# Performance work log

Hardware: AMD Instinct MI355X
Metric: run time of the kernel (lower is better)

## Reference

```python
import jax, jax.numpy as jnp
import numpy as np

DELTA_V = 0.5
DELTA_D = 3.0
ALPHA = 1.0
BETA = 1.0
GAMMA = 0.001
K = 5  # max instance label (labels 1..K; 0 = background)


def setup_inputs() -> dict:
    key = jax.random.key(0)
    k1, k2 = jax.random.split(key)
    B, D, H, W = 8, 8, 512, 1024
    embedding = jax.random.normal(k1, (B, D, H, W), dtype=jnp.float32)
    instance_mask = jax.random.randint(k2, (B, H, W), 0, K + 1, dtype=jnp.int32)
    return {"embedding": embedding, "instance_mask": instance_mask}


def _disc_loss(embedding, instance_mask):
    B, D, H, W = embedding.shape
    P = H * W
    emb = embedding.transpose(0, 2, 3, 1).reshape(B, P, D)      # [B,P,D]
    labels = instance_mask.reshape(B, P)                         # [B,P]

    # one-hot over instance labels 1..K (background excluded)
    onehot = (labels[..., None] == jnp.arange(1, K + 1, dtype=labels.dtype)).astype(emb.dtype)  # [B,P,K]
    counts = onehot.sum(axis=1)                                  # [B,K]
    present = counts > 0                                         # [B,K]
    presentf = present.astype(emb.dtype)
    N = presentf.sum(axis=-1)                                    # [B] num instances

    # per-instance centers via segment mean
    sums = jnp.einsum('bpd,bpk->bkd', emb, onehot)               # [B,K,D]
    centers = sums / jnp.maximum(counts, 1.0)[..., None]         # [B,K,D]

    # ---- variance loss: per-pixel distance to own center ----
    idx = jnp.clip(labels - 1, 0, K - 1)                         # [B,P]
    c_pix = jnp.take_along_axis(centers, idx[..., None], axis=1) # [B,P,D]
    d = jnp.sqrt(jnp.sum((emb - c_pix) ** 2, axis=-1))           # [B,P]
    val = jnp.maximum(d - DELTA_V, 0.0) ** 2                     # [B,P]
    inst_sum = jnp.einsum('bp,bpk->bk', val, onehot)             # [B,K]
    inst_mean = inst_sum / jnp.maximum(counts, 1.0)
    loss_var_b = (inst_mean * presentf).sum(-1) / jnp.maximum(N, 1.0)  # [B]

    # ---- distance loss: pairwise center hinge ----
    diff = centers[:, :, None, :] - centers[:, None, :, :]       # [B,K,K,D]
    dist_sq = jnp.sum(diff ** 2, axis=-1)                        # [B,K,K]
    iu = jnp.triu(jnp.ones((K, K), dtype=bool), k=1)             # i<j
    pair_mask = present[:, :, None] & present[:, None, :] & iu   # [B,K,K]
    safe_dist = jnp.sqrt(jnp.where(pair_mask, dist_sq, 1.0))
    term = jnp.maximum(2.0 * DELTA_D - safe_dist, 0.0) ** 2 * pair_mask.astype(emb.dtype)
    n_pairs = N * (N - 1.0) / 2.0
    loss_dist_b = term.sum((-1, -2)) / jnp.where(N > 1, n_pairs, 1.0)  # [B]

    # ---- regularization: mean norm of present centers ----
    c_norm = jnp.sqrt(jnp.where(present, jnp.sum(centers ** 2, axis=-1), 1.0))
    loss_reg_b = (c_norm * presentf).sum(-1) / jnp.maximum(N, 1.0)     # [B]

    # ---- batch mean over images that have at least one instance ----
    has = (N > 0).astype(emb.dtype)                              # [B]
    denom = jnp.maximum(has.sum(), 1.0)
    loss_var = (loss_var_b * has).sum() / denom
    loss_dist = (loss_dist_b * has).sum() / denom
    loss_reg = (loss_reg_b * has).sum() / denom
    total = ALPHA * loss_var + BETA * loss_dist + GAMMA * loss_reg
    return (total, loss_var, loss_dist, loss_reg)


def reference(embedding, instance_mask):
    return _disc_loss(embedding, instance_mask)
```

## Files before the change

### kernel.cpp

```cpp
#include <hip/hip_runtime.h>
#include <math.h>

constexpr int NB   = 8;
constexpr int ND   = 8;
constexpr int NH   = 512;
constexpr int NW   = 1024;
constexpr int NP   = NH * NW;
constexpr int NG   = NP / 4;
constexpr int NK   = 5;
constexpr int BPB  = 128;
constexpr int GPB  = NG / BPB;
constexpr int NVAL = NK * ND + NK;

constexpr float DELTA_V = 0.5f;
constexpr float TWO_DELTA_D = 6.0f;
constexpr float GAMMA = 0.001f;

__device__ __forceinline__ float wave_sum(float v) {
#pragma unroll
    for (int off = 32; off > 0; off >>= 1) v += __shfl_down(v, off, 64);
    return v;
}

__global__ __launch_bounds__(256) void pass1_kernel(const float* __restrict__ emb,
                                                    const int* __restrict__ mask,
                                                    float* __restrict__ sums,
                                                    float* __restrict__ cnts) {
    const int b   = blockIdx.x / BPB;
    const int blk = blockIdx.x % BPB;
    const long base = (long)blk * GPB;

    const float4* emb4 = (const float4*)emb;
    const int4*   m4p  = (const int4*)mask + (long)b * NG;

    float acc[NK][ND];
    float cnt[NK];
#pragma unroll
    for (int k = 0; k < NK; ++k) {
        cnt[k] = 0.f;
#pragma unroll
        for (int d = 0; d < ND; ++d) acc[k][d] = 0.f;
    }

    for (int it = threadIdx.x; it < GPB; it += blockDim.x) {
        const long g = base + it;
        const int4 m = m4p[g];
        float4 e[ND];
#pragma unroll
        for (int d = 0; d < ND; ++d)
            e[d] = emb4[((long)(b * ND + d)) * NG + g];
        const int labs[4] = {m.x, m.y, m.z, m.w};
#pragma unroll
        for (int j = 0; j < 4; ++j) {
            const int lab = labs[j];
#pragma unroll
            for (int k = 0; k < NK; ++k) {
                const float is = (lab == k + 1) ? 1.f : 0.f;
                cnt[k] += is;
#pragma unroll
                for (int d = 0; d < ND; ++d)
                    acc[k][d] = fmaf(is, ((const float*)&e[d])[j], acc[k][d]);
            }
        }
    }

    __shared__ float part[4][NVAL];
    const int lane = threadIdx.x & 63;
    const int wave = threadIdx.x >> 6;
#pragma unroll
    for (int k = 0; k < NK; ++k) {
#pragma unroll
        for (int d = 0; d < ND; ++d) {
            const float r = wave_sum(acc[k][d]);
            if (lane == 0) part[wave][k * ND + d] = r;
        }
        const float rc = wave_sum(cnt[k]);
        if (lane == 0) part[wave][NK * ND + k] = rc;
    }
    __syncthreads();
    if (threadIdx.x < NVAL) {
        const float s = part[0][threadIdx.x] + part[1][threadIdx.x] +
                        part[2][threadIdx.x] + part[3][threadIdx.x];
        if (threadIdx.x < NK * ND)
            atomicAdd(&sums[b * NK * ND + threadIdx.x], s);
        else
            atomicAdd(&cnts[b * NK + (threadIdx.x - NK * ND)], s);
    }
}

__global__ __launch_bounds__(256) void pass2_kernel(const float* __restrict__ emb,
                                                    const int* __restrict__ mask,
                                                    const float* __restrict__ sums,
                                                    const float* __restrict__ cnts,
                                                    float* __restrict__ vsums) {
    const int b   = blockIdx.x / BPB;
    const int blk = blockIdx.x % BPB;
    const long base = (long)blk * GPB;

    float c[NK][ND];
#pragma unroll
    for (int k = 0; k < NK; ++k) {
        const float inv = 1.f / fmaxf(cnts[b * NK + k], 1.f);
#pragma unroll
        for (int d = 0; d < ND; ++d)
            c[k][d] = sums[b * NK * ND + k * ND + d] * inv;
    }

    const float4* emb4 = (const float4*)emb;
    const int4*   m4p  = (const int4*)mask + (long)b * NG;

    float vacc[NK] = {0.f, 0.f, 0.f, 0.f, 0.f};

    for (int it = threadIdx.x; it < GPB; it += blockDim.x) {
        const long g = base + it;
        const int4 m = m4p[g];
        float4 e[ND];
#pragma unroll
        for (int d = 0; d < ND; ++d)
            e[d] = emb4[((long)(b * ND + d)) * NG + g];
        const int labs[4] = {m.x, m.y, m.z, m.w};
#pragma unroll
        for (int j = 0; j < 4; ++j) {
            const int lab = labs[j];
            float dsq = 0.f;
#pragma unroll
            for (int d = 0; d < ND; ++d) {
                float cd = c[0][d];
                cd = (lab == 2) ? c[1][d] : cd;
                cd = (lab == 3) ? c[2][d] : cd;
                cd = (lab == 4) ? c[3][d] : cd;
                cd = (lab == 5) ? c[4][d] : cd;
                const float diff = ((const float*)&e[d])[j] - cd;
                dsq = fmaf(diff, diff, dsq);
            }
            const float dist = sqrtf(dsq);
            float hv = fmaxf(dist - DELTA_V, 0.f);
            const float val = hv * hv;
#pragma unroll
            for (int k = 0; k < NK; ++k)
                vacc[k] += (lab == k + 1) ? val : 0.f;
        }
    }

    __shared__ float part[4][NK];
    const int lane = threadIdx.x & 63;
    const int wave = threadIdx.x >> 6;
#pragma unroll
    for (int k = 0; k < NK; ++k) {
        const float r = wave_sum(vacc[k]);
        if (lane == 0) part[wave][k] = r;
    }
    __syncthreads();
    if (threadIdx.x < NK) {
        const float s = part[0][threadIdx.x] + part[1][threadIdx.x] +
                        part[2][threadIdx.x] + part[3][threadIdx.x];
        atomicAdd(&vsums[b * NK + threadIdx.x], s);
    }
}

__global__ void final_kernel(const float* __restrict__ sums,
                             const float* __restrict__ cnts,
                             const float* __restrict__ vsums,
                             float* __restrict__ out) {
    if (threadIdx.x != 0 || blockIdx.x != 0) return;
    float tv = 0.f, td = 0.f, tr = 0.f, hs = 0.f;
    for (int b = 0; b < NB; ++b) {
        float cnt[NK];
        bool  pres[NK];
        float c[NK][ND];
        float N = 0.f;
        for (int k = 0; k < NK; ++k) {
            cnt[k]  = cnts[b * NK + k];
            pres[k] = cnt[k] > 0.f;
            if (pres[k]) N += 1.f;
            const float inv = 1.f / fmaxf(cnt[k], 1.f);
            for (int d = 0; d < ND; ++d)
                c[k][d] = sums[b * NK * ND + k * ND + d] * inv;
        }
        float lv = 0.f;
        for (int k = 0; k < NK; ++k)
            if (pres[k]) lv += vsums[b * NK + k] / fmaxf(cnt[k], 1.f);
        lv /= fmaxf(N, 1.f);
        float ld = 0.f;
        for (int i = 0; i < NK; ++i)
            for (int j = i + 1; j < NK; ++j)
                if (pres[i] && pres[j]) {
                    float dsq = 0.f;
                    for (int d = 0; d < ND; ++d) {
                        const float df = c[i][d] - c[j][d];
                        dsq = fmaf(df, df, dsq);
                    }
                    const float t = fmaxf(TWO_DELTA_D - sqrtf(dsq), 0.f);
                    ld += t * t;
                }
        const float npairs = N * (N - 1.f) * 0.5f;
        ld /= (N > 1.f) ? npairs : 1.f;
        float lr = 0.f;
        for (int k = 0; k < NK; ++k)
            if (pres[k]) {
                float sq = 0.f;
                for (int d = 0; d < ND; ++d) sq = fmaf(c[k][d], c[k][d], sq);
                lr += sqrtf(sq);
            }
        lr /= fmaxf(N, 1.f);

        if (N > 0.f) { tv += lv; td += ld; tr += lr; hs += 1.f; }
    }
    const float denom = fmaxf(hs, 1.f);
    tv /= denom; td /= denom; tr /= denom;
    out[0] = tv + td + GAMMA * tr;
    out[1] = tv;
    out[2] = td;
    out[3] = tr;
}

extern "C" void kernel_launch(void* const* d_in, const int* in_sizes, int n_in,
                              void* d_out, int out_size, void* d_ws, size_t ws_size,
                              hipStream_t stream) {
    const float* emb  = (const float*)d_in[0];
    const int*   mask = (const int*)d_in[1];
    float* out = (float*)d_out;

    float* sums  = (float*)d_ws;
    float* cnts  = sums + NB * NK * ND;
    float* vsums = cnts + NB * NK;

    hipMemsetAsync(d_ws, 0, (size_t)(NB * NK * ND + 2 * NB * NK) * sizeof(float), stream);

    dim3 grid(NB * BPB), block(256);
    pass1_kernel<<<grid, block, 0, stream>>>(emb, mask, sums, cnts);
    pass2_kernel<<<grid, block, 0, stream>>>(emb, mask, sums, cnts, vsums);
    final_kernel<<<1, 64, 0, stream>>>(sums, cnts, vsums, out);
}
```

Measured before the change: 286.1 us.

## Fuse both passes and final reduction into one cooperative kernel with grid sync

Replaces the memset plus three kernel launches with a single cooperative kernel of 512 blocks that uses grid.sync between phases. Per-block partials are written to workspace and reduced deterministically instead of through atomics. Block 0 finishes with a per-image final loss computed in parallel. This removes launch and memset overhead, but halves the block count, and grid-wide barriers add synchronisation cost. Both passes still read the embedding in full, with no reuse across them.

```diff
diff --git a/kernel.cpp b/kernel.cpp
--- a/kernel.cpp
+++ b/kernel.cpp
@@ -1,5 +1,8 @@
 #include <hip/hip_runtime.h>
+#include <hip/hip_cooperative_groups.h>
 #include <math.h>
+
+namespace cg = cooperative_groups;
 
 constexpr int NB   = 8;
 constexpr int ND   = 8;
@@ -7,14 +10,15 @@
 constexpr int NW   = 1024;
 constexpr int NP   = NH * NW;
 constexpr int NG   = NP / 4;
+constexpr int BPB  = 64;
+constexpr int NBLK = NB * BPB;
+constexpr int GPB  = NG / BPB;
 constexpr int NK   = 5;
-constexpr int BPB  = 128;
-constexpr int GPB  = NG / BPB;
 constexpr int NVAL = NK * ND + NK;
 
-constexpr float DELTA_V = 0.5f;
+constexpr float DELTA_V     = 0.5f;
 constexpr float TWO_DELTA_D = 6.0f;
-constexpr float GAMMA = 0.001f;
+constexpr float GAMMA       = 0.001f;
 
 __device__ __forceinline__ float wave_sum(float v) {
 #pragma unroll
@@ -22,17 +26,30 @@
     return v;
 }
 
-__global__ __launch_bounds__(256) void pass1_kernel(const float* __restrict__ emb,
-                                                    const int* __restrict__ mask,
-                                                    float* __restrict__ sums,
-                                                    float* __restrict__ cnts) {
+__global__ __launch_bounds__(256, 2) void fused_kernel(
+        const float* __restrict__ emb,
+        const int*   __restrict__ mask,
+        float* __restrict__ part1,
+        float* __restrict__ gcent,
+        float* __restrict__ gcnt,
+        float* __restrict__ part2,
+        float* __restrict__ out) {
+    const cg::grid_group grid = cg::this_grid();
     const int b   = blockIdx.x / BPB;
     const int blk = blockIdx.x % BPB;
     const long base = (long)blk * GPB;
+    const int lane = threadIdx.x & 63;
+    const int wave = threadIdx.x >> 6;
 
     const float4* emb4 = (const float4*)emb;
     const int4*   m4p  = (const int4*)mask + (long)b * NG;
 
+    __shared__ float part[4][NVAL];
+    __shared__ float red[NVAL];
+    __shared__ float csh[NK][ND];
+    __shared__ float vsh[NB][NK];
+    __shared__ float bl[4][NB];
+
     float acc[NK][ND];
     float cnt[NK];
 #pragma unroll
@@ -42,7 +59,7 @@
         for (int d = 0; d < ND; ++d) acc[k][d] = 0.f;
     }
 
-    for (int it = threadIdx.x; it < GPB; it += blockDim.x) {
+    for (int it = threadIdx.x; it < GPB; it += 256) {
         const long g = base + it;
         const int4 m = m4p[g];
         float4 e[ND];
@@ -64,9 +81,6 @@
         }
     }
 
-    __shared__ float part[4][NVAL];
-    const int lane = threadIdx.x & 63;
-    const int wave = threadIdx.x >> 6;
 #pragma unroll
     for (int k = 0; k < NK; ++k) {
 #pragma unroll
@@ -79,39 +93,39 @@
     }
     __syncthreads();
     if (threadIdx.x < NVAL) {
-        const float s = part[0][threadIdx.x] + part[1][threadIdx.x] +
-                        part[2][threadIdx.x] + part[3][threadIdx.x];
-        if (threadIdx.x < NK * ND)
-            atomicAdd(&sums[b * NK * ND + threadIdx.x], s);
-        else
-            atomicAdd(&cnts[b * NK + (threadIdx.x - NK * ND)], s);
-    }
-}
-
-__global__ __launch_bounds__(256) void pass2_kernel(const float* __restrict__ emb,
-                                                    const int* __restrict__ mask,
-                                                    const float* __restrict__ sums,
-                                                    const float* __restrict__ cnts,
-                                                    float* __restrict__ vsums) {
-    const int b   = blockIdx.x / BPB;
-    const int blk = blockIdx.x % BPB;
-    const long base = (long)blk * GPB;
+        part1[blockIdx.x * NVAL + threadIdx.x] =
+            part[0][threadIdx.x] + part[1][threadIdx.x] +
+            part[2][threadIdx.x] + part[3][threadIdx.x];
+    }
+
+    grid.sync();
+
+    if (threadIdx.x < NVAL) {
+        const float* p = part1 + (long)b * BPB * NVAL + threadIdx.x;
+        float s = 0.f;
+#pragma unroll 8
+        for (int i = 0; i < BPB; ++i) s += p[(long)i * NVAL];
+        red[threadIdx.x] = s;
+    }
+    __syncthreads();
+    if (threadIdx.x < NK * ND) {
+        const int k = threadIdx.x / ND;
+        const float c = red[threadIdx.x] / fmaxf(red[NK * ND + k], 1.f);
+        csh[k][threadIdx.x % ND] = c;
+        if (blk == 0) gcent[b * NK * ND + threadIdx.x] = c;
+    } else if (threadIdx.x < NVAL) {
+        if (blk == 0) gcnt[b * NK + (threadIdx.x - NK * ND)] = red[threadIdx.x];
+    }
+    __syncthreads();
 
     float c[NK][ND];
 #pragma unroll
-    for (int k = 0; k < NK; ++k) {
-        const float inv = 1.f / fmaxf(cnts[b * NK + k], 1.f);
-#pragma unroll
-        for (int d = 0; d < ND; ++d)
-            c[k][d] = sums[b * NK * ND + k * ND + d] * inv;
-    }
-
-    const float4* emb4 = (const float4*)emb;
-    const int4*   m4p  = (const int4*)mask + (long)b * NG;
+    for (int k = 0; k < NK; ++k)
+#pragma unroll
+        for (int d = 0; d < ND; ++d) c[k][d] = csh[k][d];
 
     float vacc[NK] = {0.f, 0.f, 0.f, 0.f, 0.f};
-
-    for (int it = threadIdx.x; it < GPB; it += blockDim.x) {
+    for (int it = threadIdx.x; it < GPB; it += 256) {
         const long g = base + it;
         const int4 m = m4p[g];
         float4 e[ND];
@@ -142,9 +156,6 @@
         }
     }
 
-    __shared__ float part[4][NK];
-    const int lane = threadIdx.x & 63;
-    const int wave = threadIdx.x >> 6;
 #pragma unroll
     for (int k = 0; k < NK; ++k) {
         const float r = wave_sum(vacc[k]);
@@ -152,42 +163,55 @@
     }
     __syncthreads();
     if (threadIdx.x < NK) {
-        const float s = part[0][threadIdx.x] + part[1][threadIdx.x] +
-                        part[2][threadIdx.x] + part[3][threadIdx.x];
-        atomicAdd(&vsums[b * NK + threadIdx.x], s);
-    }
-}
-
-__global__ void final_kernel(const float* __restrict__ sums,
-                             const float* __restrict__ cnts,
-                             const float* __restrict__ vsums,
-                             float* __restrict__ out) {
-    if (threadIdx.x != 0 || blockIdx.x != 0) return;
-    float tv = 0.f, td = 0.f, tr = 0.f, hs = 0.f;
-    for (int b = 0; b < NB; ++b) {
-        float cnt[NK];
+        part2[blockIdx.x * NK + threadIdx.x] =
+            part[0][threadIdx.x] + part[1][threadIdx.x] +
+            part[2][threadIdx.x] + part[3][threadIdx.x];
+    }
+
+    grid.sync();
+
+    if (blockIdx.x != 0) return;
+
+    if (threadIdx.x < NB * NK) {
+        const int bb = threadIdx.x / NK, k = threadIdx.x % NK;
+        const float* p = part2 + (long)bb * BPB * NK + k;
+        float s = 0.f;
+#pragma unroll 8
+        for (int i = 0; i < BPB; ++i) s += p[(long)i * NK];
+        vsh[bb][k] = s;
+    }
+    __syncthreads();
+
+    if (threadIdx.x < NB) {
+        const int bb = threadIdx.x;
+        float cw[NK][ND];
+        float cc[NK];
         bool  pres[NK];
-        float c[NK][ND];
         float N = 0.f;
+#pragma unroll
         for (int k = 0; k < NK; ++k) {
-            cnt[k]  = cnts[b * NK + k];
-            pres[k] = cnt[k] > 0.f;
+            cc[k]   = gcnt[bb * NK + k];
+            pres[k] = cc[k] > 0.f;
             if (pres[k]) N += 1.f;
-            const float inv = 1.f / fmaxf(cnt[k], 1.f);
+#pragma unroll
             for (int d = 0; d < ND; ++d)
-                c[k][d] = sums[b * NK * ND + k * ND + d] * inv;
+                cw[k][d] = gcent[bb * NK * ND + k * ND + d];
         }
         float lv = 0.f;
+#pragma unroll
         for (int k = 0; k < NK; ++k)
-            if (pres[k]) lv += vsums[b * NK + k] / fmaxf(cnt[k], 1.f);
+            if (pres[k]) lv += vsh[bb][k] / fmaxf(cc[k], 1.f);
         lv /= fmaxf(N, 1.f);
         float ld = 0.f;
+#pragma unroll
         for (int i = 0; i < NK; ++i)
+#pragma unroll
             for (int j = i + 1; j < NK; ++j)
                 if (pres[i] && pres[j]) {
                     float dsq = 0.f;
+#pragma unroll
                     for (int d = 0; d < ND; ++d) {
-                        const float df = c[i][d] - c[j][d];
+                        const float df = cw[i][d] - cw[j][d];
                         dsq = fmaf(df, df, dsq);
                     }
                     const float t = fmaxf(TWO_DELTA_D - sqrtf(dsq), 0.f);
@@ -196,22 +220,35 @@
         const float npairs = N * (N - 1.f) * 0.5f;
         ld /= (N > 1.f) ? npairs : 1.f;
         float lr = 0.f;
+#pragma unroll
         for (int k = 0; k < NK; ++k)
             if (pres[k]) {
                 float sq = 0.f;
-                for (int d = 0; d < ND; ++d) sq = fmaf(c[k][d], c[k][d], sq);
+#pragma unroll
+                for (int d = 0; d < ND; ++d) sq = fmaf(cw[k][d], cw[k][d], sq);
                 lr += sqrtf(sq);
             }
         lr /= fmaxf(N, 1.f);
 
-        if (N > 0.f) { tv += lv; td += ld; tr += lr; hs += 1.f; }
-    }
-    const float denom = fmaxf(hs, 1.f);
-    tv /= denom; td /= denom; tr /= denom;
-    out[0] = tv + td + GAMMA * tr;
-    out[1] = tv;
-    out[2] = td;
-    out[3] = tr;
+        const float has = (N > 0.f) ? 1.f : 0.f;
+        bl[0][bb] = lv * has;
+        bl[1][bb] = ld * has;
+        bl[2][bb] = lr * has;
+        bl[3][bb] = has;
+    }
+    __syncthreads();
+    if (threadIdx.x == 0) {
+        float tv = 0.f, td = 0.f, tr = 0.f, hs = 0.f;
+        for (int bb = 0; bb < NB; ++bb) {
+            tv += bl[0][bb]; td += bl[1][bb]; tr += bl[2][bb]; hs += bl[3][bb];
+        }
+        const float denom = fmaxf(hs, 1.f);
+        tv /= denom; td /= denom; tr /= denom;
+        out[0] = tv + td + GAMMA * tr;
+        out[1] = tv;
+        out[2] = td;
+        out[3] = tr;
+    }
 }
 
 extern "C" void kernel_launch(void* const* d_in, const int* in_sizes, int n_in,
@@ -221,14 +258,13 @@
     const int*   mask = (const int*)d_in[1];
     float* out = (float*)d_out;
 
-    float* sums  = (float*)d_ws;
-    float* cnts  = sums + NB * NK * ND;
-    float* vsums = cnts + NB * NK;
-
-    hipMemsetAsync(d_ws, 0, (size_t)(NB * NK * ND + 2 * NB * NK) * sizeof(float), stream);
-
-    dim3 grid(NB * BPB), block(256);
-    pass1_kernel<<<grid, block, 0, stream>>>(emb, mask, sums, cnts);
-    pass2_kernel<<<grid, block, 0, stream>>>(emb, mask, sums, cnts, vsums);
-    final_kernel<<<1, 64, 0, stream>>>(sums, cnts, vsums, out);
+    float* part1 = (float*)d_ws;
+    float* gcent = part1 + NBLK * NVAL;
+    float* gcnt  = gcent + NB * NK * ND;
+    float* part2 = gcnt  + NB * NK;
+
+    void* args[] = { (void*)&emb, (void*)&mask, (void*)&part1, (void*)&gcent,
+                     (void*)&gcnt, (void*)&part2, (void*)&out };
+    hipLaunchCooperativeKernel((const void*)fused_kernel, dim3(NBLK), dim3(256),
+                               args, 0, stream);
 }
```

Result: slower. 347.5 us (+21.5%).
